# Kernel tuning notes

Measured on AMD Instinct MI355X. Metric: run time of the kernel, lower is better.

The kernel has to match this reference:

```python
import jax, jax.numpy as jnp
import numpy as np

B, CI, H, W = 128, 16, 32, 32
CO, K, S = 32, 3, 1
HO = (H - K) // S + 1  # 30
WO = (W - K) // S + 1  # 30
P = HO * WO  # 900 spatial locations
B_J0 = 0.1
DT = 0.5
BETA_ADAPT = 1.8  # is_adapt=True
BN_EPS = 1e-5


def setup_inputs() -> dict:
    key = jax.random.key(0)
    ks = jax.random.split(key, 16)
    inp = {
        'ff': jax.random.normal(ks[0], (B, CI, H, W), jnp.float32),
        'fb': jax.random.normal(ks[1], (B, CO, HO, WO), jnp.float32),
        'soma_t': jax.random.normal(ks[2], (B, CO, HO, WO), jnp.float32),
        'spk_t': (jax.random.uniform(ks[3], (B, CO, HO, WO)) > 0.7).astype(jnp.float32),
        'a_curr_t': jax.random.normal(ks[4], (B, CO, HO, WO), jnp.float32),
        'b_t': jax.random.uniform(ks[5], (B, CO, HO, WO), jnp.float32),
        # parameters
        'weight': jax.random.normal(ks[6], (1, CO, CI, HO, WO, K * K), jnp.float32) * 0.05,
        'conv_bias': jnp.zeros((1, CO, HO, WO), jnp.float32),
        'local_rec': jax.random.normal(ks[7], (P, CO, CO), jnp.float32) * (1.0 / np.sqrt(2.0 * CO)),
        'gamma': jnp.ones((CO,), jnp.float32),
        'beta': jnp.zeros((CO,), jnp.float32),
        'tau_m': 15.0 + 0.1 * jax.random.normal(ks[8], (CO, HO, WO), jnp.float32),
        'tau_adp': 20.0 + 0.1 * jax.random.normal(ks[9], (CO, HO, WO), jnp.float32),
        'tau_a': 15.0 + 0.1 * jax.random.normal(ks[10], (CO, HO, WO), jnp.float32),
    }
    return inp


def local_conv(x, weight, bias):
    # torch unfold(2,k).unfold(3,k) order: (kh, kw) fastest -> [B,Ci,Ho,Wo,k*k]
    patches = jnp.stack(
        [x[:, :, i:i + S * HO:S, j:j + S * WO:S] for i in range(K) for j in range(K)],
        axis=-1)
    out = jnp.einsum('bchwk,ochwk->bohw', patches, weight[0])
    return out + bias


def reference(ff, fb, soma_t, spk_t, a_curr_t, b_t, weight, conv_bias,
              local_rec, gamma, beta, tau_m, tau_adp, tau_a):
    # locally-connected conv + BatchNorm2d (training mode: batch stats)
    conv = local_conv(ff, weight, conv_bias)
    mean = conv.mean(axis=(0, 2, 3), keepdims=True)
    var = ((conv - mean) ** 2).mean(axis=(0, 2, 3), keepdims=True)  # biased var
    x = (conv - mean) * jax.lax.rsqrt(var + BN_EPS)
    conv_x = x * gamma[None, :, None, None] + beta[None, :, None, None]
    # recurrent per-location bmm: local_rec [P,Co,Co] @ spk [P,Co,B]
    spk_flat = spk_t.reshape(B, CO, P)
    rec = jnp.einsum('pij,bjp->bip', local_rec, spk_flat).reshape(B, CO, HO, WO)
    conv_x = conv_x + rec
    # adaptive LIF membrane update
    alpha = jnp.exp(-DT / tau_m)
    rho = jnp.exp(-DT / tau_adp)
    eta = jnp.exp(-DT / tau_a)
    b_new = rho * b_t + (1.0 - rho) * spk_t
    new_thre = B_J0 + BETA_ADAPT * b_new
    a_new = eta * a_curr_t + fb
    soma_new = alpha * soma_t + (jax.nn.sigmoid(a_new) - 0.5) + conv_x - new_thre * spk_t
    spike = (soma_new - new_thre > 0).astype(soma_new.dtype)
    return soma_new, spike, a_new, b_new
```

## Files before the change

kernel.cpp:

```cpp
#include <hip/hip_runtime.h>
#include <math.h>

#pragma clang fp contract(off)

#define B_   128
#define CI_  16
#define CO_  32
#define H_   32
#define W_   32
#define HO_  30
#define WO_  30
#define P_   900
#define CP_  (CO_*P_)
#define N_   ((size_t)B_*CP_)
#define NBLK_CONV (4*30*8)
#define WSTRIDE_O 129600
#define WSTRIDE_C 8100
#define FFC_ (H_*W_)
#define FFB_ (CI_*H_*W_)
#define FFTOT_ (B_*FFB_)


typedef __attribute__((address_space(1))) const unsigned int gas_uint;
typedef __attribute__((address_space(3))) unsigned int las_uint;
__device__ __forceinline__ void gload_lds4(const float* g, float* l) {
    __builtin_amdgcn_global_load_lds((gas_uint*)g, (las_uint*)l, 4, 0, 0);
}
__device__ __forceinline__ void gload_lds16(const float* g, float* l) {
    __builtin_amdgcn_global_load_lds((gas_uint*)g, (las_uint*)l, 16, 0, 0);
}

__global__ __launch_bounds__(128) void conv_kernel(
    const float* __restrict__ ff, const float* __restrict__ weight,
    const float* __restrict__ conv_bias, float* __restrict__ outf,
    double* __restrict__ part_sum, double* __restrict__ part_sumsq)
{
#pragma clang fp contract(off)
    const int tid = threadIdx.x;
    const int og  = (tid & 3) | ((tid >> 6) << 2);
    const int wg2 = (tid >> 2) & 3;
    const int bg  = (tid >> 4) & 3;
    const int wave = tid >> 6;
    const int wt = blockIdx.x & 3;
    const int os = blockIdx.x >> 2;
    const int h  = blockIdx.y;
    const int b0 = blockIdx.z * 16;
    const int w0 = wt * 8 + wg2 * 2;
    const bool val = !(wt == 3 && wg2 == 3);
    const int wwave = tid & ~63;

    __shared__ float wgl[2][1344];
    __shared__ float ffs[2][576];

    int wq_off[8];
#pragma unroll
    for (int q = 0; q < 8; ++q) {
        int s = q * 128 + tid;
        int ol = s >> 6, w = (s >> 3) & 7, k = s & 7;
        int colc = wt * 8 + w; if (colc > 29) colc = 29;
        wq_off[q] = (os * 16 + ol) * WSTRIDE_O + (h * WO_ + colc) * 9 + k;
    }
    int w8_off;
    {
        int ol = tid >> 3, w = tid & 7;
        int colc = wt * 8 + w; if (colc > 29) colc = 29;
        w8_off = (os * 16 + ol) * WSTRIDE_O + (h * WO_ + colc) * 9 + 8;
    }
    int f_off, f_off2 = 0;
    {
        int s0 = 4 * tid;
        int bb = s0 / 36, rm = s0 % 36, r = rm / 12, cc0 = rm % 12;
        f_off = (b0 + bb) * FFB_ + (h + r) * W_ + wt * 8 + cc0;
    }
    const bool f2on = (tid < 16);
    if (f2on) {
        int s0 = 512 + 4 * tid;
        int bb = s0 / 36, rm = s0 % 36, r = rm / 12, cc0 = rm % 12;
        f_off2 = (b0 + bb) * FFB_ + (h + r) * W_ + wt * 8 + cc0;
    }

    float acc[2][2][4];
#pragma unroll
    for (int oo = 0; oo < 2; ++oo)
#pragma unroll
        for (int ww = 0; ww < 2; ++ww)
#pragma unroll
            for (int j = 0; j < 4; ++j) acc[oo][ww][j] = 0.f;

    auto stage = [&](int c, int buf) {
        const float* wsrc = weight + c * WSTRIDE_C;
#pragma unroll
        for (int q = 0; q < 8; ++q)
            gload_lds4(wsrc + wq_off[q], &wgl[buf][(2 * q + wave) * 76]);
        gload_lds4(wsrc + w8_off, &wgl[buf][1216 + (wave << 6)]);
        {
            int g = f_off + c * FFC_;
            if (g > FFTOT_ - 4) g = FFTOT_ - 4;
            gload_lds16(ff + g, &ffs[buf][4 * wwave]);
        }
        if (f2on) {
            int g = f_off2 + c * FFC_;
            if (g > FFTOT_ - 4) g = FFTOT_ - 4;
            gload_lds16(ff + g, &ffs[buf][512]);
        }
    };

    auto compute_c = [&](int buf) {
        float wk[2][2][9];
#pragma unroll
        for (int oo = 0; oo < 2; ++oo)
#pragma unroll
            for (int ww = 0; ww < 2; ++ww) {
                const int ol = oo * 8 + og, w = wg2 * 2 + ww;
                const float* wp = &wgl[buf][ol * 76 + w * 8];
                const float4 a = *reinterpret_cast<const float4*>(wp);
                const float4 b = *reinterpret_cast<const float4*>(wp + 4);
                wk[oo][ww][0] = a.x; wk[oo][ww][1] = a.y; wk[oo][ww][2] = a.z; wk[oo][ww][3] = a.w;
                wk[oo][ww][4] = b.x; wk[oo][ww][5] = b.y; wk[oo][ww][6] = b.z; wk[oo][ww][7] = b.w;
                wk[oo][ww][8] = wgl[buf][1216 + ol * 8 + w];
            }
#pragma unroll
        for (int j = 0; j < 4; ++j) {
            const int bb = bg * 4 + j;
            float fr[3][4];
#pragma unroll
            for (int r = 0; r < 3; ++r) {
                const float2 u = *reinterpret_cast<const float2*>(&ffs[buf][bb * 36 + r * 12 + wg2 * 2]);
                const float2 v = *reinterpret_cast<const float2*>(&ffs[buf][bb * 36 + r * 12 + wg2 * 2 + 2]);
                fr[r][0] = u.x; fr[r][1] = u.y; fr[r][2] = v.x; fr[r][3] = v.y;
            }
#pragma unroll
            for (int oo = 0; oo < 2; ++oo)
#pragma unroll
                for (int ww = 0; ww < 2; ++ww) {
                    float a = acc[oo][ww][j];
#pragma unroll
                    for (int kh = 0; kh < 3; ++kh)
#pragma unroll
                        for (int kw = 0; kw < 3; ++kw) {
                            float prod = wk[oo][ww][kh * 3 + kw] * fr[kh][ww + kw];
                            a = a + prod;
                        }
                    acc[oo][ww][j] = a;
                }
        }
    };

    stage(0, 0);
    __syncthreads();
    for (int cs = 0; cs < CI_; cs += 2) {
        if (cs + 1 < CI_) stage(cs + 1, 1);
        compute_c(0);
        __syncthreads();
        if (cs + 2 < CI_) stage(cs + 2, 0);
        compute_c(1);
        __syncthreads();
    }

    double s1[2] = {0.0, 0.0}, s2[2] = {0.0, 0.0};
    if (val) {
#pragma unroll
        for (int oo = 0; oo < 2; ++oo) {
            const int o = os * 16 + oo * 8 + og;
            const int pidx = o * P_ + h * WO_ + w0;
            const float2 bi = *reinterpret_cast<const float2*>(conv_bias + pidx);
#pragma unroll
            for (int j = 0; j < 4; ++j) {
                const int b = b0 + bg * 4 + j;
                const size_t n = (size_t)b * CP_ + (size_t)pidx;
                float v0 = acc[oo][0][j] + bi.x;
                float v1 = acc[oo][1][j] + bi.y;
                *reinterpret_cast<float2*>(outf + 3 * N_ + n) = make_float2(v0, v1);
                double d0 = (double)v0, d1 = (double)v1;
                s1[oo] += d0; s2[oo] += d0 * d0;
                s1[oo] += d1; s2[oo] += d1 * d1;
            }
        }
    }
#pragma unroll
    for (int d = 4; d < 64; d <<= 1) {
#pragma unroll
        for (int oo = 0; oo < 2; ++oo) {
            s1[oo] += __shfl_xor(s1[oo], d);
            s2[oo] += __shfl_xor(s2[oo], d);
        }
    }
    if ((tid & 60) == 0) {
        int blk = (blockIdx.z * 30 + blockIdx.y) * 4 + wt;
#pragma unroll
        for (int oo = 0; oo < 2; ++oo) {
            const int o = os * 16 + oo * 8 + og;
            part_sum  [blk * CO_ + o] = s1[oo];
            part_sumsq[blk * CO_ + o] = s2[oo];
        }
    }
}

__global__ __launch_bounds__(256) void bn_finalize(
    const double* __restrict__ part_sum, const double* __restrict__ part_sumsq,
    float* __restrict__ Mb)
{
#pragma clang fp contract(off)
    const int o = blockIdx.x;
    const int tid = threadIdx.x;
    double s1 = 0.0, s2 = 0.0;
    for (int i = tid; i < NBLK_CONV; i += 256) {
        s1 += part_sum[i * CO_ + o];
        s2 += part_sumsq[i * CO_ + o];
    }
    __shared__ double r1[256], r2[256];
    r1[tid] = s1; r2[tid] = s2;
    __syncthreads();
    for (int s = 128; s > 0; s >>= 1) {
        if (tid < s) { r1[tid] += r1[tid + s]; r2[tid] += r2[tid + s]; }
        __syncthreads();
    }
    if (tid == 0) {
        const double cnt = (double)(B_ * (size_t)P_);
        double mean = r1[0] / cnt;
        float meanf = (float)mean;
        double md = (double)meanf;
        double var = r2[0] / cnt - 2.0 * md * (r1[0] / cnt) + md * md;
        float varf = (float)var;
        float invf = 1.0f / sqrtf(varf + 1e-5f);
        Mb[o]       = meanf;
        Mb[CO_ + o] = invf;
    }
}

__global__ __launch_bounds__(1024) void lif_rec_kernel(
    float* __restrict__ outf, const float* __restrict__ local_rec,
    const float* __restrict__ tau_m, const float* __restrict__ tau_adp,
    const float* __restrict__ tau_a, const float* __restrict__ Mb,
    const float* __restrict__ gamma, const float* __restrict__ beta,
    const float* __restrict__ fb, const float* __restrict__ soma_t,
    const float* __restrict__ spk_t, const float* __restrict__ a_curr,
    const float* __restrict__ b_t)
{
#pragma clang fp contract(off)
    const int D    = blockIdx.x;
    const int pt8  = D & 7;
    const int rest = D >> 3;
    const int by   = rest & 15;
    const int ptq  = rest >> 4;
    const int pt   = ptq * 8 + pt8;
    if (pt >= 29) return;

    const int tid = threadIdx.x;
    const int pp  = tid & 31;
    const int i   = tid >> 5;
    const int p   = pt * 32 + pp;
    const bool pv = (p < P_);
    const int b0  = by * 8;

    float L[32];
    float meanf = 0.f, invf = 0.f, gm = 0.f, be = 0.f;
    float al = 0.f, rh = 0.f, et = 0.f;
    int rem = 0;
    if (pv) {
        const float4* lp = reinterpret_cast<const float4*>(local_rec + (size_t)p * (CO_ * CO_) + i * CO_);
#pragma unroll
        for (int q = 0; q < 8; ++q) {
            float4 v = lp[q];
            L[4 * q] = v.x; L[4 * q + 1] = v.y; L[4 * q + 2] = v.z; L[4 * q + 3] = v.w;
        }
        rem = i * P_ + p;
        meanf = Mb[i]; invf = Mb[CO_ + i];
        gm = gamma[i]; be = beta[i];
        al = expf(-0.5f / tau_m[rem]);
        rh = expf(-0.5f / tau_adp[rem]);
        et = expf(-0.5f / tau_a[rem]);
    }
    const float omr = 1.0f - rh;

    __shared__ float sp[4][CO_][32];

    size_t n = (size_t)b0 * CP_ + (size_t)rem;
    float sk0 = 0.f, cv0 = 0.f, bt0 = 0.f, ac0 = 0.f, fb0 = 0.f, so0 = 0.f;
    float sk1 = 0.f, cv1 = 0.f, bt1 = 0.f, ac1 = 0.f, fb1 = 0.f, so1 = 0.f;
    if (pv) {
        sk0 = spk_t[n];       cv0 = outf[3 * N_ + n];       bt0 = b_t[n];
        ac0 = a_curr[n];      fb0 = fb[n];                  so0 = soma_t[n];
        const size_t n1 = n + (size_t)CP_;
        sk1 = spk_t[n1];      cv1 = outf[3 * N_ + n1];      bt1 = b_t[n1];
        ac1 = a_curr[n1];     fb1 = fb[n1];                 so1 = soma_t[n1];
    }

#pragma unroll
    for (int r = 0; r < 4; ++r) {
        const int t0 = (r & 1) * 2;
        if (pv) {
            sp[t0][i][pp]     = sk0;
            sp[t0 + 1][i][pp] = sk1;
        }
        float sk0n = 0.f, cv0n = 0.f, bt0n = 0.f, ac0n = 0.f, fb0n = 0.f, so0n = 0.f;
        float sk1n = 0.f, cv1n = 0.f, bt1n = 0.f, ac1n = 0.f, fb1n = 0.f, so1n = 0.f;
        if (r < 3 && pv) {
            const size_t n2 = n + (size_t)(2 * CP_);
            const size_t n3 = n + (size_t)(3 * CP_);
            sk0n = spk_t[n2];  cv0n = outf[3 * N_ + n2];  bt0n = b_t[n2];
            ac0n = a_curr[n2]; fb0n = fb[n2];             so0n = soma_t[n2];
            sk1n = spk_t[n3];  cv1n = outf[3 * N_ + n3];  bt1n = b_t[n3];
            ac1n = a_curr[n3]; fb1n = fb[n3];             so1n = soma_t[n3];
        }
        asm volatile("s_waitcnt lgkmcnt(0)\n\ts_barrier" ::: "memory");
        if (pv) {
            {
                float rec = 0.f;
#pragma unroll
                for (int j = 0; j < CO_; ++j) {
                    float prod = L[j] * sp[t0][j][pp];
                    rec = rec + prod;
                }
                float t  = cv0 - meanf;
                float x  = t * invf;
                float xg = x * gm;
                float cx = xg + be;
                cx = cx + rec;
                float rb  = rh * bt0;
                float os  = omr * sk0;
                float bn  = rb + os;
                float tb = 1.8f * bn;
                float th = 0.1f + tb;
                float ea = et * ac0;
                float an = ea + fb0;
                float sg = 1.0f / (1.0f + expf(-an));
                float as = al * so0;
                float s5 = sg - 0.5f;
                float u1 = as + s5;
                float u2 = u1 + cx;
                float ts = th * sk0;
                float sn = u2 - ts;
                outf[n]          = sn;
                outf[N_ + n]     = ((sn - th) > 0.0f) ? 1.f : 0.f;
                outf[2 * N_ + n] = an;
                outf[3 * N_ + n] = bn;
            }
            {
                const size_t n1 = n + (size_t)CP_;
                float rec = 0.f;
#pragma unroll
                for (int j = 0; j < CO_; ++j) {
                    float prod = L[j] * sp[t0 + 1][j][pp];
                    rec = rec + prod;
                }
                float t  = cv1 - meanf;
                float x  = t * invf;
                float xg = x * gm;
                float cx = xg + be;
                cx = cx + rec;
                float rb  = rh * bt1;
                float os  = omr * sk1;
                float bn  = rb + os;
                float tb = 1.8f * bn;
                float th = 0.1f + tb;
                float ea = et * ac1;
                float an = ea + fb1;
                float sg = 1.0f / (1.0f + expf(-an));
                float as = al * so1;
                float s5 = sg - 0.5f;
                float u1 = as + s5;
                float u2 = u1 + cx;
                float ts = th * sk1;
                float sn = u2 - ts;
                outf[n1]          = sn;
                outf[N_ + n1]     = ((sn - th) > 0.0f) ? 1.f : 0.f;
                outf[2 * N_ + n1] = an;
                outf[3 * N_ + n1] = bn;
            }
        }
        sk0 = sk0n; cv0 = cv0n; bt0 = bt0n; ac0 = ac0n; fb0 = fb0n; so0 = so0n;
        sk1 = sk1n; cv1 = cv1n; bt1 = bt1n; ac1 = ac1n; fb1 = fb1n; so1 = so1n;
        n += (size_t)(2 * CP_);
    }
}

extern "C" void kernel_launch(void* const* d_in, const int* in_sizes, int n_in,
                              void* d_out, int out_size, void* d_ws, size_t ws_size,
                              hipStream_t stream)
{
    const float* ff        = (const float*)d_in[0];
    const float* fb        = (const float*)d_in[1];
    const float* soma_t    = (const float*)d_in[2];
    const float* spk_t     = (const float*)d_in[3];
    const float* a_curr    = (const float*)d_in[4];
    const float* b_t       = (const float*)d_in[5];
    const float* weight    = (const float*)d_in[6];
    const float* conv_bias = (const float*)d_in[7];
    const float* local_rec = (const float*)d_in[8];
    const float* gamma     = (const float*)d_in[9];
    const float* beta      = (const float*)d_in[10];
    const float* tau_m     = (const float*)d_in[11];
    const float* tau_adp   = (const float*)d_in[12];
    const float* tau_a     = (const float*)d_in[13];

    double* part_sum = (double*)d_ws;
    double* part_sq  = part_sum + (size_t)NBLK_CONV * CO_;
    float*  Mb       = (float*)(part_sq + (size_t)NBLK_CONV * CO_);

    float* outf = (float*)d_out;

    conv_kernel<<<dim3(8, 30, 8), 128, 0, stream>>>(
        ff, weight, conv_bias, outf, part_sum, part_sq);
    bn_finalize<<<dim3(CO_), 256, 0, stream>>>(part_sum, part_sq, Mb);
    lif_rec_kernel<<<dim3(512), 1024, 0, stream>>>(
        outf, local_rec, tau_m, tau_adp, tau_a, Mb, gamma, beta,
        fb, soma_t, spk_t, a_curr, b_t);
}
```

Before: 105.2 us.

## Split conv blocks into single-wave blocks covering 8 output channels

Shrinks the conv kernel's blocks from two waves (16 output channels) to one wave (8 output channels) and doubles the grid along x. Weight and input staging into LDS is rewritten for 64 threads, with more global-to-LDS loads per thread. The goal is more, smaller blocks to improve occupancy and scheduling across CUs. The cost is that each ff input tile is now loaded twice as often, since it is shared by fewer channels per block.

```diff
diff --git a/kernel.cpp b/kernel.cpp
--- a/kernel.cpp
+++ b/kernel.cpp
@@ -30,53 +30,53 @@
     __builtin_amdgcn_global_load_lds((gas_uint*)g, (las_uint*)l, 16, 0, 0);
 }
 
-__global__ __launch_bounds__(128) void conv_kernel(
+__global__ __launch_bounds__(64) void conv_kernel(
     const float* __restrict__ ff, const float* __restrict__ weight,
     const float* __restrict__ conv_bias, float* __restrict__ outf,
     double* __restrict__ part_sum, double* __restrict__ part_sumsq)
 {
 #pragma clang fp contract(off)
     const int tid = threadIdx.x;
-    const int og  = (tid & 3) | ((tid >> 6) << 2);
+    const int og  = tid & 3;
     const int wg2 = (tid >> 2) & 3;
     const int bg  = (tid >> 4) & 3;
-    const int wave = tid >> 6;
-    const int wt = blockIdx.x & 3;
-    const int os = blockIdx.x >> 2;
-    const int h  = blockIdx.y;
-    const int b0 = blockIdx.z * 16;
-    const int w0 = wt * 8 + wg2 * 2;
+    const int wt  = blockIdx.x & 3;
+    const int os  = blockIdx.x >> 2;
+    const int h   = blockIdx.y;
+    const int b0  = blockIdx.z * 16;
+    const int w0  = wt * 8 + wg2 * 2;
     const bool val = !(wt == 3 && wg2 == 3);
-    const int wwave = tid & ~63;
-
-    __shared__ float wgl[2][1344];
+    const int ob  = os * 8;
+
+    __shared__ float wgl[2][672];
     __shared__ float ffs[2][576];
 
-    int wq_off[8];
-#pragma unroll
-    for (int q = 0; q < 8; ++q) {
-        int s = q * 128 + tid;
-        int ol = s >> 6, w = (s >> 3) & 7, k = s & 7;
-        int colc = wt * 8 + w; if (colc > 29) colc = 29;
-        wq_off[q] = (os * 16 + ol) * WSTRIDE_O + (h * WO_ + colc) * 9 + k;
-    }
-    int w8_off;
-    {
-        int ol = tid >> 3, w = tid & 7;
-        int colc = wt * 8 + w; if (colc > 29) colc = 29;
-        w8_off = (os * 16 + ol) * WSTRIDE_O + (h * WO_ + colc) * 9 + 8;
-    }
-    int f_off, f_off2 = 0;
-    {
-        int s0 = 4 * tid;
-        int bb = s0 / 36, rm = s0 % 36, r = rm / 12, cc0 = rm % 12;
-        f_off = (b0 + bb) * FFB_ + (h + r) * W_ + wt * 8 + cc0;
-    }
-    const bool f2on = (tid < 16);
-    if (f2on) {
-        int s0 = 512 + 4 * tid;
-        int bb = s0 / 36, rm = s0 % 36, r = rm / 12, cc0 = rm % 12;
-        f_off2 = (b0 + bb) * FFB_ + (h + r) * W_ + wt * 8 + cc0;
+    int wq_off[11];
+#pragma unroll
+    for (int q = 0; q < 11; ++q) {
+        int m = q * 64 + tid;
+        int src = 0;
+        if (m < 608) {
+            int ol = m / 76, r = m - ol * 76;
+            if (r < 64) {
+                int w = r >> 3, k = r & 7;
+                int colc = wt * 8 + w; if (colc > 29) colc = 29;
+                src = (ob + ol) * WSTRIDE_O + (h * WO_ + colc) * 9 + k;
+            }
+        } else if (m < 672) {
+            int idx = m - 608, ol = idx >> 3, w = idx & 7;
+            int colc = wt * 8 + w; if (colc > 29) colc = 29;
+            src = (ob + ol) * WSTRIDE_O + (h * WO_ + colc) * 9 + 8;
+        }
+        wq_off[q] = src;
+    }
+    int f_off[3];
+#pragma unroll
+    for (int q = 0; q < 3; ++q) {
+        int d = q * 256 + tid * 4;
+        int dd = (d < 576) ? d : 0;
+        int bb = dd / 36, rm = dd - bb * 36, r = rm / 12, cc0 = rm - r * 12;
+        f_off[q] = (b0 + bb) * FFB_ + (h + r) * W_ + wt * 8 + cc0;
     }
 
     float acc[2][2][4];
@@ -90,18 +90,17 @@
     auto stage = [&](int c, int buf) {
         const float* wsrc = weight + c * WSTRIDE_C;
 #pragma unroll
-        for (int q = 0; q < 8; ++q)
-            gload_lds4(wsrc + wq_off[q], &wgl[buf][(2 * q + wave) * 76]);
-        gload_lds4(wsrc + w8_off, &wgl[buf][1216 + (wave << 6)]);
-        {
-            int g = f_off + c * FFC_;
-            if (g > FFTOT_ - 4) g = FFTOT_ - 4;
-            gload_lds16(ff + g, &ffs[buf][4 * wwave]);
-        }
-        if (f2on) {
-            int g = f_off2 + c * FFC_;
-            if (g > FFTOT_ - 4) g = FFTOT_ - 4;
-            gload_lds16(ff + g, &ffs[buf][512]);
+        for (int q = 0; q < 10; ++q)
+            gload_lds4(wsrc + wq_off[q], &wgl[buf][q * 64]);
+        if (tid < 32)
+            gload_lds4(wsrc + wq_off[10], &wgl[buf][640]);
+#pragma unroll
+        for (int q = 0; q < 3; ++q) {
+            if (q < 2 || tid < 16) {
+                int g = f_off[q] + c * FFC_;
+                if (g > FFTOT_ - 4) g = FFTOT_ - 4;
+                gload_lds16(ff + g, &ffs[buf][q * 256]);
+            }
         }
     };
 
@@ -111,13 +110,13 @@
         for (int oo = 0; oo < 2; ++oo)
 #pragma unroll
             for (int ww = 0; ww < 2; ++ww) {
-                const int ol = oo * 8 + og, w = wg2 * 2 + ww;
+                const int ol = oo * 4 + og, w = wg2 * 2 + ww;
                 const float* wp = &wgl[buf][ol * 76 + w * 8];
                 const float4 a = *reinterpret_cast<const float4*>(wp);
                 const float4 b = *reinterpret_cast<const float4*>(wp + 4);
                 wk[oo][ww][0] = a.x; wk[oo][ww][1] = a.y; wk[oo][ww][2] = a.z; wk[oo][ww][3] = a.w;
                 wk[oo][ww][4] = b.x; wk[oo][ww][5] = b.y; wk[oo][ww][6] = b.z; wk[oo][ww][7] = b.w;
-                wk[oo][ww][8] = wgl[buf][1216 + ol * 8 + w];
+                wk[oo][ww][8] = wgl[buf][608 + ol * 8 + w];
             }
 #pragma unroll
         for (int j = 0; j < 4; ++j) {
@@ -161,7 +160,7 @@
     if (val) {
 #pragma unroll
         for (int oo = 0; oo < 2; ++oo) {
-            const int o = os * 16 + oo * 8 + og;
+            const int o = ob + oo * 4 + og;
             const int pidx = o * P_ + h * WO_ + w0;
             const float2 bi = *reinterpret_cast<const float2*>(conv_bias + pidx);
 #pragma unroll
@@ -189,7 +188,7 @@
         int blk = (blockIdx.z * 30 + blockIdx.y) * 4 + wt;
 #pragma unroll
         for (int oo = 0; oo < 2; ++oo) {
-            const int o = os * 16 + oo * 8 + og;
+            const int o = ob + oo * 4 + og;
             part_sum  [blk * CO_ + o] = s1[oo];
             part_sumsq[blk * CO_ + o] = s2[oo];
         }
@@ -400,7 +399,7 @@
 
     float* outf = (float*)d_out;
 
-    conv_kernel<<<dim3(8, 30, 8), 128, 0, stream>>>(
+    conv_kernel<<<dim3(16, 30, 8), 64, 0, stream>>>(
         ff, weight, conv_bias, outf, part_sum, part_sq);
     bn_finalize<<<dim3(CO_), 256, 0, stream>>>(part_sum, part_sq, Mb);
     lif_rec_kernel<<<dim3(512), 1024, 0, stream>>>(
```

After: 104.6 us. Within noise of the previous version (-0.6%).
